# Kernel optimization log

Measured on AMD Instinct MI355X. Metric: run time of the kernel, lower is better.

Reference implementation:

```python
import jax, jax.numpy as jnp
import numpy as np

UFEAT_DIM = 512
EFEAT_DIM = 256
BATCH = 64
PNUM_UNIT = 1024
PNUM_ENEMY = 1024


def setup_inputs() -> dict:
    key = jax.random.key(0)
    k1, k2, k3, k4, k5 = jax.random.split(key, 5)
    ufeat = jax.random.normal(k1, (BATCH, PNUM_UNIT, UFEAT_DIM), dtype=jnp.float32)
    efeat = jax.random.normal(k2, (BATCH, PNUM_ENEMY, EFEAT_DIM), dtype=jnp.float32)
    num_enemy = jax.random.randint(k3, (BATCH,), 0, PNUM_ENEMY, dtype=jnp.int64)
    # weight_norm(Linear, dim=None): W = g * v / ||v||_F, g scalar
    v = jax.random.normal(k4, (EFEAT_DIM, UFEAT_DIM), dtype=jnp.float32) * (1.0 / np.sqrt(UFEAT_DIM))
    g = jnp.asarray(jnp.linalg.norm(v), dtype=jnp.float32)  # init g = ||v||
    b = jax.random.normal(k5, (EFEAT_DIM,), dtype=jnp.float32) * 0.01
    return {"ufeat": ufeat, "efeat": efeat, "num_enemy": num_enemy, "v": v, "g": g, "b": b}


def reference(ufeat, efeat, num_enemy, v, g, b):
    # weight-normed linear (dim=None -> Frobenius norm) + ReLU projection
    W = g * v / jnp.linalg.norm(v)                       # [efeat_dim, ufeat_dim]
    proj = jax.nn.relu(ufeat @ W.T + b)                  # [B, U, efeat_dim]
    # batched dot-product scores (fused matmul instead of repeat+mul+sum)
    norm = jnp.float32(np.sqrt(EFEAT_DIM))
    logit = jnp.einsum('bue,bne->bun', proj, efeat) / norm  # [B, U, N]
    # real-enemy mask: mask[b, n] = 1 iff n < num_enemy[b]
    mask = (jnp.arange(PNUM_ENEMY)[None, :] < num_enemy[:, None]).astype(logit.dtype)
    logit = logit - (1.0 - mask)[:, None, :] * 1e9       # masking bias (uniform if all masked)
    prob = jax.nn.softmax(logit, axis=2)
    return prob
```

## Files before the change

kernel.cpp:

```cpp
#include <hip/hip_runtime.h>
#include <hip/hip_bf16.h>

#define UF 512
#define EF 256
#define NB 64
#define NU 1024
#define NEN 1024

typedef __attribute__((ext_vector_type(8))) short short8;
typedef __attribute__((ext_vector_type(4))) float floatx4;

typedef unsigned short ushort_t;

__device__ inline short2 cvt2(float a, float b) {
    __hip_bfloat162 h = __float22bfloat162_rn(make_float2(a, b));
    union { __hip_bfloat162 h; short2 s; } u;
    u.h = h;
    return u.s;
}

__device__ inline short8 cvt8v(floatx4 x, floatx4 y) {
    union { short8 v; short2 s[4]; } u;
    u.s[0] = cvt2(x[0], x[1]);
    u.s[1] = cvt2(x[2], x[3]);
    u.s[2] = cvt2(y[0], y[1]);
    u.s[3] = cvt2(y[2], y[3]);
    return u.v;
}

__device__ inline ushort_t f2bfbits(float f) {
    unsigned u = __float_as_uint(f);
    u += 0x7FFFu + ((u >> 16) & 1u);
    return (ushort_t)(u >> 16);
}

__global__ void knorm(const float* __restrict__ v, float* __restrict__ ws0) {
    int t = blockIdx.x * 256 + threadIdx.x;
    float2 x = ((const float2*)v)[t];
    float s = x.x * x.x + x.y * x.y;
    #pragma unroll
    for (int m = 1; m < 64; m <<= 1) s += __shfl_xor(s, m);
    __shared__ float ls[4];
    int w = threadIdx.x >> 6;
    if ((threadIdx.x & 63) == 0) ls[w] = s;
    __syncthreads();
    if (threadIdx.x == 0) atomicAdd(ws0, ls[0] + ls[1] + ls[2] + ls[3]);
}

__global__ void kconv(const float* __restrict__ v, const float* __restrict__ g,
                      const float* __restrict__ ef, const float* __restrict__ ws0,
                      const int* __restrict__ nen,
                      ushort_t* __restrict__ wsW, ushort_t* __restrict__ wsE) {
    int bid = blockIdx.x;
    if (bid < 128) {
        int t = bid * 256 + threadIdx.x;
        float s = g[0] * rsqrtf(ws0[0]);
        float4 x = ((const float4*)v)[t];
        short2 a = cvt2(x.x * s, x.y * s);
        short2 b = cvt2(x.z * s, x.w * s);
        ushort4 o;
        o.x = (ushort_t)a.x; o.y = (ushort_t)a.y; o.z = (ushort_t)b.x; o.w = (ushort_t)b.y;
        ((ushort4*)wsW)[t] = o;
    } else {
        long t = (long)(bid - 128) * 256 + threadIdx.x;
        int row = (int)(t >> 6);
        int n = row & (NEN - 1);
        int b = row >> 10;
        if (n < nen[b]) {
            float4 x = ((const float4*)ef)[t];
            short2 a = cvt2(x.x, x.y);
            short2 c = cvt2(x.z, x.w);
            ushort4 o;
            o.x = (ushort_t)a.x; o.y = (ushort_t)a.y; o.z = (ushort_t)c.x; o.w = (ushort_t)c.y;
            ((ushort4*)wsE)[t] = o;
        }
    }
}

__launch_bounds__(256, 2)
__global__ void kgemm1(const float* __restrict__ A, const ushort_t* __restrict__ W,
                       const float* __restrict__ bias, ushort_t* __restrict__ P) {
    const int tid = threadIdx.x;
    const int wv = tid >> 6, L = tid & 63;
    const int rA = L & 15, q = L >> 4;
    const int mh = wv >> 1;
    const int nh = wv & 1;
    const long m0 = (long)blockIdx.x * 64 + mh * 32;

    floatx4 acc[2][8];
    #pragma unroll
    for (int m = 0; m < 2; m++)
        #pragma unroll
        for (int n = 0; n < 8; n++) acc[m][n] = (floatx4){0.f, 0.f, 0.f, 0.f};

    const float* a0 = A + (m0 + rA) * UF + q * 8;
    const float* a1 = A + (m0 + 16 + rA) * UF + q * 8;
    const ushort_t* wb = W + (long)(nh * 128 + rA) * UF + q * 8;

    floatx4 x0 = *(const floatx4*)(a0);
    floatx4 y0 = *(const floatx4*)(a0 + 4);
    floatx4 x1 = *(const floatx4*)(a1);
    floatx4 y1 = *(const floatx4*)(a1 + 4);

    #pragma unroll 2
    for (int s = 0; s < 16; s++) {
        const int ko = s * 32;
        short8 wf[8];
        #pragma unroll
        for (int n = 0; n < 8; n++) wf[n] = *(const short8*)(wb + (long)n * 16 * UF + ko);
        short8 af0 = cvt8v(x0, y0);
        short8 af1 = cvt8v(x1, y1);
        if (s < 15) {
            x0 = *(const floatx4*)(a0 + ko + 32);
            y0 = *(const floatx4*)(a0 + ko + 36);
            x1 = *(const floatx4*)(a1 + ko + 32);
            y1 = *(const floatx4*)(a1 + ko + 36);
        }
        #pragma unroll
        for (int n = 0; n < 8; n++) {
            acc[0][n] = __builtin_amdgcn_mfma_f32_16x16x32_bf16(af0, wf[n], acc[0][n], 0, 0, 0);
            acc[1][n] = __builtin_amdgcn_mfma_f32_16x16x32_bf16(af1, wf[n], acc[1][n], 0, 0, 0);
        }
    }

    #pragma unroll
    for (int n = 0; n < 8; n++) {
        const int col = nh * 128 + n * 16 + rA;
        const float bv = bias[col];
        #pragma unroll
        for (int m = 0; m < 2; m++) {
            #pragma unroll
            for (int i = 0; i < 4; i++) {
                float val = acc[m][n][i] + bv;
                val = fmaxf(val, 0.f);
                const long row = m0 + m * 16 + q * 4 + i;
                P[row * EF + col] = f2bfbits(val);
            }
        }
    }
}

__launch_bounds__(256, 2)
__global__ void kattn(const ushort_t* __restrict__ P, const ushort_t* __restrict__ E,
                      const int* __restrict__ nen, float* __restrict__ out) {
    const int tid = threadIdx.x;
    const int w = tid >> 6, L = tid & 63;
    const int rA = L & 15, q = L >> 4;
    const int bid = blockIdx.x;
    const int b = bid >> 5;
    const int ut = bid & 31;
    const int ne = nen[b];

    const ushort_t* prow = P + (long)(b * NU + ut * 32 + rA) * EF + q * 8;
    short8 af[2][8];
    #pragma unroll
    for (int t = 0; t < 2; t++)
        #pragma unroll
        for (int s = 0; s < 8; s++)
            af[t][s] = *(const short8*)(prow + t * 16 * EF + s * 32);

    floatx4 acc[2][16];
    #pragma unroll
    for (int t = 0; t < 2; t++)
        #pragma unroll
        for (int ns = 0; ns < 16; ns++) acc[t][ns] = (floatx4){0.f, 0.f, 0.f, 0.f};
    float psum[2][4];
    #pragma unroll
    for (int t = 0; t < 2; t++)
        #pragma unroll
        for (int i = 0; i < 4; i++) psum[t][i] = 0.f;

    const ushort_t* erow = E + (long)(b * NEN + w * 16 + rA) * EF + q * 8;

    #pragma unroll
    for (int ns = 0; ns < 16; ns++) {
        const int col0 = ns * 64 + w * 16;
        if (col0 < ne) {
            const ushort_t* ep = erow + (long)ns * 64 * EF;
            floatx4 c0 = (floatx4){0.f, 0.f, 0.f, 0.f};
            floatx4 c1 = (floatx4){0.f, 0.f, 0.f, 0.f};
            #pragma unroll
            for (int h = 0; h < 2; h++) {
                short8 bf[4];
                #pragma unroll
                for (int s = 0; s < 4; s++) bf[s] = *(const short8*)(ep + (h * 4 + s) * 32);
                #pragma unroll
                for (int s = 0; s < 4; s++) {
                    c0 = __builtin_amdgcn_mfma_f32_16x16x32_bf16(af[0][h * 4 + s], bf[s], c0, 0, 0, 0);
                    c1 = __builtin_amdgcn_mfma_f32_16x16x32_bf16(af[1][h * 4 + s], bf[s], c1, 0, 0, 0);
                }
            }
            const int col = col0 + rA;
            const bool on = col < ne;
            #pragma unroll
            for (int i = 0; i < 4; i++) {
                float e0 = on ? __expf(c0[i] * 0.0625f) : 0.f;
                float e1 = on ? __expf(c1[i] * 0.0625f) : 0.f;
                c0[i] = e0; c1[i] = e1;
                psum[0][i] += e0; psum[1][i] += e1;
            }
            acc[0][ns] = c0;
            acc[1][ns] = c1;
        }
    }

    #pragma unroll
    for (int t = 0; t < 2; t++)
        #pragma unroll
        for (int i = 0; i < 4; i++) {
            float s = psum[t][i];
            s += __shfl_xor(s, 1);
            s += __shfl_xor(s, 2);
            s += __shfl_xor(s, 4);
            s += __shfl_xor(s, 8);
            psum[t][i] = s;
        }
    __shared__ float lsum[4][32];
    if (rA == 0) {
        #pragma unroll
        for (int t = 0; t < 2; t++)
            #pragma unroll
            for (int i = 0; i < 4; i++)
                lsum[w][t * 16 + q * 4 + i] = psum[t][i];
    }
    __syncthreads();

    float inv[2][4];
    #pragma unroll
    for (int t = 0; t < 2; t++)
        #pragma unroll
        for (int i = 0; i < 4; i++) {
            const int r = t * 16 + q * 4 + i;
            const float tot = lsum[0][r] + lsum[1][r] + lsum[2][r] + lsum[3][r];
            inv[t][i] = (ne > 0) ? (1.f / tot) : 0.f;
        }

    const float uni = 1.f / 1024.f;
    float* orow = out + ((long)(b * NU + ut * 32)) * (long)NEN + w * 16;
    #pragma unroll
    for (int ns = 0; ns < 16; ns++) {
        #pragma unroll
        for (int t = 0; t < 2; t++) {
            #pragma unroll
            for (int i = 0; i < 4; i++) {
                const int u = t * 16 + q * 4 + i;
                const float val = (ne == 0) ? uni : acc[t][ns][i] * inv[t][i];
                __builtin_nontemporal_store(val, &orow[(long)u * NEN + ns * 64 + rA]);
            }
        }
    }
}

extern "C" void kernel_launch(void* const* d_in, const int* in_sizes, int n_in,
                              void* d_out, int out_size, void* d_ws, size_t ws_size,
                              hipStream_t stream) {
    (void)in_sizes; (void)n_in; (void)out_size; (void)ws_size;
    const float* ufeat = (const float*)d_in[0];
    const float* efeat = (const float*)d_in[1];
    const int*   nen   = (const int*)d_in[2];
    const float* v     = (const float*)d_in[3];
    const float* g     = (const float*)d_in[4];
    const float* bias  = (const float*)d_in[5];
    float* out = (float*)d_out;

    float*    ws0 = (float*)d_ws;
    ushort_t* wsW = (ushort_t*)((char*)d_ws + 1024);
    ushort_t* wsE = (ushort_t*)((char*)d_ws + (1u << 20));
    ushort_t* wsP = (ushort_t*)((char*)d_ws + (1u << 20) + (32u << 20));

    hipMemsetAsync(d_ws, 0, 256, stream);
    knorm<<<256, 256, 0, stream>>>(v, ws0);
    kconv<<<16512, 256, 0, stream>>>(v, g, efeat, ws0, nen, wsW, wsE);
    kgemm1<<<1024, 256, 0, stream>>>(ufeat, wsW, bias, wsP);
    kattn<<<2048, 256, 0, stream>>>(wsP, wsE, nen, out);
}
```

Before: 575.1 us.

## Fuse projection GEMM into attention kernel via shared-memory P tile

Merges the projection GEMM kernel into the attention kernel. Each block now computes its 32-row bf16 projection tile into LDS and consumes it directly, so the P intermediate no longer takes a global write and read-back and one launch is dropped. In exchange, each block re-reads all of W (256x512 bf16) from global/L2, and the 16KB LDS tile may reduce occupancy. The efeat conversion load is also made nontemporal.

New measurement: 569.2 us. No clear change (-1.0%).

```diff
diff --git a/kernel.cpp b/kernel.cpp
--- a/kernel.cpp
+++ b/kernel.cpp
@@ -67,9 +67,9 @@
         int n = row & (NEN - 1);
         int b = row >> 10;
         if (n < nen[b]) {
-            float4 x = ((const float4*)ef)[t];
-            short2 a = cvt2(x.x, x.y);
-            short2 c = cvt2(x.z, x.w);
+            floatx4 x = __builtin_nontemporal_load((const floatx4*)ef + t);
+            short2 a = cvt2(x[0], x[1]);
+            short2 c = cvt2(x[2], x[3]);
             ushort4 o;
             o.x = (ushort_t)a.x; o.y = (ushort_t)a.y; o.z = (ushort_t)c.x; o.w = (ushort_t)c.y;
             ((ushort4*)wsE)[t] = o;
@@ -78,71 +78,9 @@
 }
 
 __launch_bounds__(256, 2)
-__global__ void kgemm1(const float* __restrict__ A, const ushort_t* __restrict__ W,
-                       const float* __restrict__ bias, ushort_t* __restrict__ P) {
-    const int tid = threadIdx.x;
-    const int wv = tid >> 6, L = tid & 63;
-    const int rA = L & 15, q = L >> 4;
-    const int mh = wv >> 1;
-    const int nh = wv & 1;
-    const long m0 = (long)blockIdx.x * 64 + mh * 32;
-
-    floatx4 acc[2][8];
-    #pragma unroll
-    for (int m = 0; m < 2; m++)
-        #pragma unroll
-        for (int n = 0; n < 8; n++) acc[m][n] = (floatx4){0.f, 0.f, 0.f, 0.f};
-
-    const float* a0 = A + (m0 + rA) * UF + q * 8;
-    const float* a1 = A + (m0 + 16 + rA) * UF + q * 8;
-    const ushort_t* wb = W + (long)(nh * 128 + rA) * UF + q * 8;
-
-    floatx4 x0 = *(const floatx4*)(a0);
-    floatx4 y0 = *(const floatx4*)(a0 + 4);
-    floatx4 x1 = *(const floatx4*)(a1);
-    floatx4 y1 = *(const floatx4*)(a1 + 4);
-
-    #pragma unroll 2
-    for (int s = 0; s < 16; s++) {
-        const int ko = s * 32;
-        short8 wf[8];
-        #pragma unroll
-        for (int n = 0; n < 8; n++) wf[n] = *(const short8*)(wb + (long)n * 16 * UF + ko);
-        short8 af0 = cvt8v(x0, y0);
-        short8 af1 = cvt8v(x1, y1);
-        if (s < 15) {
-            x0 = *(const floatx4*)(a0 + ko + 32);
-            y0 = *(const floatx4*)(a0 + ko + 36);
-            x1 = *(const floatx4*)(a1 + ko + 32);
-            y1 = *(const floatx4*)(a1 + ko + 36);
-        }
-        #pragma unroll
-        for (int n = 0; n < 8; n++) {
-            acc[0][n] = __builtin_amdgcn_mfma_f32_16x16x32_bf16(af0, wf[n], acc[0][n], 0, 0, 0);
-            acc[1][n] = __builtin_amdgcn_mfma_f32_16x16x32_bf16(af1, wf[n], acc[1][n], 0, 0, 0);
-        }
-    }
-
-    #pragma unroll
-    for (int n = 0; n < 8; n++) {
-        const int col = nh * 128 + n * 16 + rA;
-        const float bv = bias[col];
-        #pragma unroll
-        for (int m = 0; m < 2; m++) {
-            #pragma unroll
-            for (int i = 0; i < 4; i++) {
-                float val = acc[m][n][i] + bv;
-                val = fmaxf(val, 0.f);
-                const long row = m0 + m * 16 + q * 4 + i;
-                P[row * EF + col] = f2bfbits(val);
-            }
-        }
-    }
-}
-
-__launch_bounds__(256, 2)
-__global__ void kattn(const ushort_t* __restrict__ P, const ushort_t* __restrict__ E,
-                      const int* __restrict__ nen, float* __restrict__ out) {
+__global__ void kfused(const float* __restrict__ A, const ushort_t* __restrict__ W,
+                       const float* __restrict__ bias, const ushort_t* __restrict__ E,
+                       const int* __restrict__ nen, float* __restrict__ out) {
     const int tid = threadIdx.x;
     const int w = tid >> 6, L = tid & 63;
     const int rA = L & 15, q = L >> 4;
@@ -151,13 +89,72 @@
     const int ut = bid & 31;
     const int ne = nen[b];
 
-    const ushort_t* prow = P + (long)(b * NU + ut * 32 + rA) * EF + q * 8;
+    __shared__ ushort_t Pl[32][256];
+    __shared__ float lsum[4][32];
+
+    {
+        const long m0 = (long)b * NU + (long)ut * 32;
+        floatx4 acc[2][4];
+        #pragma unroll
+        for (int m = 0; m < 2; m++)
+            #pragma unroll
+            for (int n = 0; n < 4; n++) acc[m][n] = (floatx4){0.f, 0.f, 0.f, 0.f};
+
+        const float* a0 = A + (m0 + rA) * UF + q * 8;
+        const float* a1 = A + (m0 + 16 + rA) * UF + q * 8;
+        const ushort_t* wp[4];
+        #pragma unroll
+        for (int n = 0; n < 4; n++) wp[n] = W + (long)(w * 64 + n * 16 + rA) * UF + q * 8;
+
+        floatx4 x0 = *(const floatx4*)(a0);
+        floatx4 y0 = *(const floatx4*)(a0 + 4);
+        floatx4 x1 = *(const floatx4*)(a1);
+        floatx4 y1 = *(const floatx4*)(a1 + 4);
+
+        #pragma unroll 2
+        for (int s = 0; s < 16; s++) {
+            const int ko = s * 32;
+            short8 wf[4];
+            #pragma unroll
+            for (int n = 0; n < 4; n++) wf[n] = *(const short8*)(wp[n] + ko);
+            short8 af0 = cvt8v(x0, y0);
+            short8 af1 = cvt8v(x1, y1);
+            if (s < 15) {
+                x0 = *(const floatx4*)(a0 + ko + 32);
+                y0 = *(const floatx4*)(a0 + ko + 36);
+                x1 = *(const floatx4*)(a1 + ko + 32);
+                y1 = *(const floatx4*)(a1 + ko + 36);
+            }
+            #pragma unroll
+            for (int n = 0; n < 4; n++) {
+                acc[0][n] = __builtin_amdgcn_mfma_f32_16x16x32_bf16(af0, wf[n], acc[0][n], 0, 0, 0);
+                acc[1][n] = __builtin_amdgcn_mfma_f32_16x16x32_bf16(af1, wf[n], acc[1][n], 0, 0, 0);
+            }
+        }
+
+        #pragma unroll
+        for (int n = 0; n < 4; n++) {
+            const int col = w * 64 + n * 16 + rA;
+            const float bv = bias[col];
+            #pragma unroll
+            for (int m = 0; m < 2; m++) {
+                #pragma unroll
+                for (int i = 0; i < 4; i++) {
+                    float val = acc[m][n][i] + bv;
+                    val = fmaxf(val, 0.f);
+                    Pl[m * 16 + q * 4 + i][col] = f2bfbits(val);
+                }
+            }
+        }
+    }
+    __syncthreads();
+
     short8 af[2][8];
     #pragma unroll
     for (int t = 0; t < 2; t++)
         #pragma unroll
         for (int s = 0; s < 8; s++)
-            af[t][s] = *(const short8*)(prow + t * 16 * EF + s * 32);
+            af[t][s] = *(const short8*)&Pl[t * 16 + rA][s * 32 + q * 8];
 
     floatx4 acc[2][16];
     #pragma unroll
@@ -215,7 +212,6 @@
             s += __shfl_xor(s, 8);
             psum[t][i] = s;
         }
-    __shared__ float lsum[4][32];
     if (rA == 0) {
         #pragma unroll
         for (int t = 0; t < 2; t++)
@@ -266,11 +262,9 @@
     float*    ws0 = (float*)d_ws;
     ushort_t* wsW = (ushort_t*)((char*)d_ws + 1024);
     ushort_t* wsE = (ushort_t*)((char*)d_ws + (1u << 20));
-    ushort_t* wsP = (ushort_t*)((char*)d_ws + (1u << 20) + (32u << 20));
 
     hipMemsetAsync(d_ws, 0, 256, stream);
     knorm<<<256, 256, 0, stream>>>(v, ws0);
     kconv<<<16512, 256, 0, stream>>>(v, g, efeat, ws0, nen, wsW, wsE);
-    kgemm1<<<1024, 256, 0, stream>>>(ufeat, wsW, bias, wsP);
-    kattn<<<2048, 256, 0, stream>>>(wsP, wsE, nen, out);
-}
+    kfused<<<2048, 256, 0, stream>>>(ufeat, wsW, bias, wsE, nen, out);
+}
```
